# Kernel optimization log

Measured on AMD Instinct MI355X. Metric: run time of the kernel, lower is better.

Reference implementation:

```python
import jax, jax.numpy as jnp
import numpy as np

THRESH = 0.1        # Huber threshold (self.threshold)
CORR_WT = 1.0       # corr_wt
ENTROPY_WT = 0.0001 # entropy_wt
BS, N = 32, 1024    # n_pts = nv = 1024 hardcoded in multi_pose_with_pts


def setup_inputs() -> dict:
    key = jax.random.key(0)
    ks = jax.random.split(key, 7)
    return {
        "points_1": jax.random.normal(ks[0], (BS, N, 3), jnp.float32),
        "points_2": jax.random.normal(ks[1], (BS, N, 3), jnp.float32),
        "assign_mat_1": jax.random.normal(ks[2], (BS, N, N), jnp.float32),
        "assign_mat_2": jax.random.normal(ks[3], (BS, N, N), jnp.float32),
        "scale": jax.random.uniform(ks[4], (BS,), jnp.float32, 0.5, 1.5),
        "rotation": jax.random.normal(ks[5], (BS, 3, 3), jnp.float32),
        "translation": jax.random.normal(ks[6], (BS, 3), jnp.float32),
    }


def _transform(sRt, pts):
    # apply 4x4 pose to [b, n, 3] points (homogeneous, keep xyz)
    return jnp.einsum('bij,bnj->bni', sRt[:, :3, :3], pts) + sRt[:, :3, 3][:, None, :]


def _chamfer(x, y):
    # squared pairwise distances [b, n, m]; loss = mean min both directions
    d = (jnp.sum(x * x, -1)[:, :, None] + jnp.sum(y * y, -1)[:, None, :]
         - 2.0 * jnp.einsum('bnd,bmd->bnm', x, y))
    d = jnp.maximum(d, 0.0)
    return jnp.mean(jnp.min(d, axis=2)) + jnp.mean(jnp.min(d, axis=1))


def _corr(a, b):
    # smooth-L1-like (Huber) correspondence loss
    diff = jnp.abs(a - b)
    loss = jnp.where(diff > THRESH, diff - THRESH / 2.0, diff * diff / (2.0 * THRESH))
    return CORR_WT * jnp.mean(jnp.sum(loss, axis=2))


def _entropy(assign_mat, soft_assign, axis):
    log_assign = jax.nn.log_softmax(assign_mat, axis=axis)
    return ENTROPY_WT * jnp.mean(-jnp.sum(soft_assign * log_assign, axis=axis))


def _cos_loss(m1, m2, eps=1e-8):
    a = m1.reshape(m1.shape[0], -1)
    b = m2.reshape(m2.shape[0], -1)
    na = jnp.maximum(jnp.linalg.norm(a, axis=1), eps)
    nb = jnp.maximum(jnp.linalg.norm(b, axis=1), eps)
    return jnp.mean(1.0 - jnp.sum(a * b, axis=1) / (na * nb))


def reference(points_1, points_2, assign_mat_1, assign_mat_2, scale, rotation, translation):
    sa1 = jax.nn.softmax(assign_mat_1, axis=2)
    sa2 = jax.nn.softmax(assign_mat_2, axis=2)

    # pose_dict_RT: sRt = [[s*R, t], [0, 1]]
    sR = rotation * scale[:, None, None]
    sRt = jnp.concatenate([sR, translation[:, :, None]], axis=2)          # b 3 4
    bottom = jnp.broadcast_to(jnp.array([0., 0., 0., 1.], sRt.dtype), (sRt.shape[0], 1, 4))
    sRt12 = jnp.concatenate([sRt, bottom], axis=1)                        # b 4 4
    sRt21 = jnp.linalg.inv(sRt12)

    p1in2 = jnp.einsum('bnm,bmd->bnd', sa1, points_2)
    p2in1 = jnp.einsum('bnm,bmd->bnd', sa2, points_1)
    p1to2 = _transform(sRt12, points_1)
    p2to1 = _transform(sRt21, points_2)

    cd1 = _chamfer(p1to2, p1in2)
    cd2 = _chamfer(p2to1, p2in1)
    total = (cd1 + cd2
             + _corr(p1in2, p1to2) + _corr(p2in1, p2to1)
             + _entropy(assign_mat_1, sa1, 2) + _entropy(assign_mat_2, sa2, 2)
             + _cos_loss(assign_mat_1, assign_mat_2)
             + _entropy(assign_mat_1, sa1, 1) + _entropy(assign_mat_2, sa2, 1))
    return total
```

## Files before the change

kernel.cpp:

```cpp
#include <hip/hip_runtime.h>
#include <math.h>

#define BSZ 32
#define NP  1024

#define OFF_ACC   0
#define OFF_COS   8
#define OFF_POSE  104
#define OFF_P1IN2 872
#define OFF_P2IN1 (OFF_P1IN2 + 3 * BSZ * NP)
#define OFF_COLP  (OFF_P2IN1 + 3 * BSZ * NP)

__global__ void k_pose(const float* __restrict__ scale,
                       const float* __restrict__ rot,
                       const float* __restrict__ tr,
                       float* __restrict__ ws) {
    int t = threadIdx.x;
    if (t < 52) {
        ws[OFF_ACC + 2 * t]     = 0.f;
        ws[OFF_ACC + 2 * t + 1] = 0.f;
    }
    if (t >= BSZ) return;
    int b = t;
    float s = scale[b];
    float M[9];
#pragma unroll
    for (int i = 0; i < 9; ++i) M[i] = rot[b * 9 + i] * s;
    float t0 = tr[b * 3 + 0], t1 = tr[b * 3 + 1], t2 = tr[b * 3 + 2];
    float det = M[0] * (M[4] * M[8] - M[5] * M[7])
              - M[1] * (M[3] * M[8] - M[5] * M[6])
              + M[2] * (M[3] * M[7] - M[4] * M[6]);
    float id = 1.0f / det;
    float inv[9];
    inv[0] =  (M[4] * M[8] - M[5] * M[7]) * id;
    inv[1] = -(M[1] * M[8] - M[2] * M[7]) * id;
    inv[2] =  (M[1] * M[5] - M[2] * M[4]) * id;
    inv[3] = -(M[3] * M[8] - M[5] * M[6]) * id;
    inv[4] =  (M[0] * M[8] - M[2] * M[6]) * id;
    inv[5] = -(M[0] * M[5] - M[2] * M[3]) * id;
    inv[6] =  (M[3] * M[7] - M[4] * M[6]) * id;
    inv[7] = -(M[0] * M[7] - M[1] * M[6]) * id;
    inv[8] =  (M[0] * M[4] - M[1] * M[3]) * id;
    float u0 = -(inv[0] * t0 + inv[1] * t1 + inv[2] * t2);
    float u1 = -(inv[3] * t0 + inv[4] * t1 + inv[5] * t2);
    float u2 = -(inv[6] * t0 + inv[7] * t1 + inv[8] * t2);
    float* P = ws + OFF_POSE + b * 24;
#pragma unroll
    for (int i = 0; i < 9; ++i) P[i] = M[i];
    P[9] = t0; P[10] = t1; P[11] = t2;
#pragma unroll
    for (int i = 0; i < 9; ++i) P[12 + i] = inv[i];
    P[21] = u0; P[22] = u1; P[23] = u2;
}

__global__ __launch_bounds__(256) void k_big(
    const float* __restrict__ am1, const float* __restrict__ am2,
    const float* __restrict__ pts1, const float* __restrict__ pts2,
    float* __restrict__ p1in2, float* __restrict__ p2in1,
    float* __restrict__ colPart, float* __restrict__ cosacc, float* __restrict__ acc) {
    __shared__ float cacc[4096];
    __shared__ float ptsL[6144];
    const int b  = blockIdx.x >> 5;
    const int rb = blockIdx.x & 31;
    const int wv = threadIdx.x >> 6;
    const int ln = threadIdx.x & 63;
    const int row0 = rb * 32 + wv * 8;

    for (int i = threadIdx.x; i < 4096; i += 256) cacc[i] = 0.f;
    for (int t = threadIdx.x; t < 6144; t += 256) {
        int mat = t >= 3072;
        int loc = t - mat * 3072;
        int c = loc / 3, d = loc - 3 * c;
        float v = mat ? pts1[b * 3072 + loc] : pts2[b * 3072 + loc];
        ptsL[mat * 3072 + d * 1024 + 256 * (c & 3) + (c >> 2)] = v;
    }
    __syncthreads();

    float C1[16], T1[16], C2[16], T2[16];
#pragma unroll
    for (int i = 0; i < 16; ++i) { C1[i] = 0.f; T1[i] = 0.f; C2[i] = 0.f; T2[i] = 0.f; }
    float dacc = 0.f, n1a = 0.f, n2a = 0.f, e2a = 0.f, sSa = 0.f;

    const float4* rA = (const float4*)(am1 + ((size_t)b * NP + row0) * NP);
    const float4* rB = (const float4*)(am2 + ((size_t)b * NP + row0) * NP);

#pragma unroll 1
    for (int r = 0; r < 8; ++r) {
        float4 a[4], c4[4];
#pragma unroll
        for (int j = 0; j < 4; ++j) {
            a[j]  = rA[(size_t)r * 256 + ln + 64 * j];
            c4[j] = rB[(size_t)r * 256 + ln + 64 * j];
        }
#pragma unroll
        for (int j = 0; j < 4; ++j) {
            dacc += a[j].x * c4[j].x + a[j].y * c4[j].y + a[j].z * c4[j].z + a[j].w * c4[j].w;
            n1a  += a[j].x * a[j].x + a[j].y * a[j].y + a[j].z * a[j].z + a[j].w * a[j].w;
            n2a  += c4[j].x * c4[j].x + c4[j].y * c4[j].y + c4[j].z * c4[j].z + c4[j].w * c4[j].w;
        }
        {
            float R = 0.f, Su = 0.f, q0 = 0.f, q1 = 0.f, q2 = 0.f;
#pragma unroll
            for (int j = 0; j < 4; ++j) {
                float* e = (float*)&a[j];
#pragma unroll
                for (int k = 0; k < 4; ++k) {
                    int i = 4 * j + k;
                    int pidx = 256 * k + 64 * j + ln;
                    float v  = e[k];
                    float ex = __expf(v);
                    R += ex; Su += ex * v;
                    q0 += ex * ptsL[pidx];
                    q1 += ex * ptsL[1024 + pidx];
                    q2 += ex * ptsL[2048 + pidx];
                    C1[i] += ex;
                    e[k] = ex;
                }
            }
#pragma unroll
            for (int m = 1; m < 64; m <<= 1) {
                R  += __shfl_xor(R, m);  Su += __shfl_xor(Su, m);
                q0 += __shfl_xor(q0, m); q1 += __shfl_xor(q1, m); q2 += __shfl_xor(q2, m);
            }
            float inv = 1.0f / R;
#pragma unroll
            for (int j = 0; j < 4; ++j) {
                float* e = (float*)&a[j];
#pragma unroll
                for (int k = 0; k < 4; ++k) T1[4 * j + k] += e[k] * inv;
            }
            float S = Su * inv;
            if (ln == 0) {
                e2a += __logf(R) - S;
                sSa += S;
                int row = b * NP + row0 + r;
                p1in2[row * 3 + 0] = q0 * inv;
                p1in2[row * 3 + 1] = q1 * inv;
                p1in2[row * 3 + 2] = q2 * inv;
            }
        }
        {
            float R = 0.f, Su = 0.f, q0 = 0.f, q1 = 0.f, q2 = 0.f;
#pragma unroll
            for (int j = 0; j < 4; ++j) {
                float* e = (float*)&c4[j];
#pragma unroll
                for (int k = 0; k < 4; ++k) {
                    int i = 4 * j + k;
                    int pidx = 3072 + 256 * k + 64 * j + ln;
                    float v  = e[k];
                    float ex = __expf(v);
                    R += ex; Su += ex * v;
                    q0 += ex * ptsL[pidx];
                    q1 += ex * ptsL[1024 + pidx];
                    q2 += ex * ptsL[2048 + pidx];
                    C2[i] += ex;
                    e[k] = ex;
                }
            }
#pragma unroll
            for (int m = 1; m < 64; m <<= 1) {
                R  += __shfl_xor(R, m);  Su += __shfl_xor(Su, m);
                q0 += __shfl_xor(q0, m); q1 += __shfl_xor(q1, m); q2 += __shfl_xor(q2, m);
            }
            float inv = 1.0f / R;
#pragma unroll
            for (int j = 0; j < 4; ++j) {
                float* e = (float*)&c4[j];
#pragma unroll
                for (int k = 0; k < 4; ++k) T2[4 * j + k] += e[k] * inv;
            }
            float S = Su * inv;
            if (ln == 0) {
                e2a += __logf(R) - S;
                sSa += S;
                int row = b * NP + row0 + r;
                p2in1[row * 3 + 0] = q0 * inv;
                p2in1[row * 3 + 1] = q1 * inv;
                p2in1[row * 3 + 2] = q2 * inv;
            }
        }
    }

#pragma unroll
    for (int j = 0; j < 4; ++j)
#pragma unroll
        for (int k = 0; k < 4; ++k) {
            int i = 4 * j + k;
            int c = 256 * j + 4 * ln + k;
            atomicAdd(&cacc[c],        C1[i]);
            atomicAdd(&cacc[1024 + c], T1[i]);
            atomicAdd(&cacc[2048 + c], C2[i]);
            atomicAdd(&cacc[3072 + c], T2[i]);
        }
#pragma unroll
    for (int m = 1; m < 64; m <<= 1) {
        dacc += __shfl_xor(dacc, m);
        n1a  += __shfl_xor(n1a, m);
        n2a  += __shfl_xor(n2a, m);
    }
    if (ln == 0) {
        atomicAdd(&cosacc[b], dacc);
        atomicAdd(&cosacc[32 + b], n1a);
        atomicAdd(&cosacc[64 + b], n2a);
        atomicAdd(&acc[0], e2a);
        atomicAdd(&acc[1], sSa);
    }
    __syncthreads();
    float4* cp = (float4*)(colPart + (size_t)blockIdx.x * 4096);
    const float4* cs = (const float4*)cacc;
    for (int i = threadIdx.x; i < 1024; i += 256) cp[i] = cs[i];
}

__global__ void k_colred(const float* __restrict__ colPart, float* __restrict__ acc) {
    int idx = blockIdx.x * 256 + threadIdx.x;
    int b = idx >> 11;
    int m = (idx >> 10) & 1;
    int c = idx & 1023;
    const float* p = colPart + (size_t)b * 32 * 4096 + m * 2048 + c;
    float C = 0.f, T = 0.f;
#pragma unroll
    for (int rbi = 0; rbi < 32; ++rbi) {
        C += p[rbi * 4096];
        T += p[rbi * 4096 + 1024];
    }
    float v = T * __logf(C);
#pragma unroll
    for (int mm = 1; mm < 64; mm <<= 1) v += __shfl_xor(v, mm);
    if ((threadIdx.x & 63) == 0) atomicAdd(&acc[2], v);
}

__global__ __launch_bounds__(256) void k_cham(
    const float* __restrict__ p1, const float* __restrict__ p2,
    const float* __restrict__ p1in2, const float* __restrict__ p2in1,
    const float* __restrict__ pose, float* __restrict__ acc) {
    __shared__ float4 ys[NP];
    const int blk   = blockIdx.x;
    const int chunk = blk & 3;
    const int b     = (blk >> 2) & 31;
    const int dir   = (blk >> 7) & 1;
    const int pair  = blk >> 8;
    const float* P   = pose + b * 24 + pair * 12;
    const float* raw = pair ? p2 : p1;
    const float* inA = pair ? p2in1 : p1in2;
    const int t = threadIdx.x;

    float m0 = P[0], m1 = P[1], m2 = P[2];
    float m3 = P[3], m4 = P[4], m5 = P[5];
    float m6 = P[6], m7 = P[7], m8 = P[8];
    float t0 = P[9], t1 = P[10], t2 = P[11];

#pragma unroll
    for (int i = 0; i < 4; ++i) {
        int q = t + 256 * i;
        int gi = (b * NP + q) * 3;
        float x, y, z;
        if (dir == 0) { x = inA[gi]; y = inA[gi + 1]; z = inA[gi + 2]; }
        else {
            float rx = raw[gi], ry = raw[gi + 1], rz = raw[gi + 2];
            x = m0 * rx + m1 * ry + m2 * rz + t0;
            y = m3 * rx + m4 * ry + m5 * rz + t1;
            z = m6 * rx + m7 * ry + m8 * rz + t2;
        }
        ys[q] = make_float4(x, y, z, x * x + y * y + z * z);
    }
    __syncthreads();

    int xi = chunk * 256 + t;
    int gx = (b * NP + xi) * 3;
    float x0, x1, x2;
    if (dir == 0) {
        float rx = raw[gx], ry = raw[gx + 1], rz = raw[gx + 2];
        x0 = m0 * rx + m1 * ry + m2 * rz + t0;
        x1 = m3 * rx + m4 * ry + m5 * rz + t1;
        x2 = m6 * rx + m7 * ry + m8 * rz + t2;
    } else { x0 = inA[gx]; x1 = inA[gx + 1]; x2 = inA[gx + 2]; }
    float sx = x0 * x0 + x1 * x1 + x2 * x2;

    float mn = 3.0e38f;
#pragma unroll 4
    for (int o = 0; o < NP; ++o) {
        float4 yv = ys[o];
        float d = fmaf(-2.0f, x0 * yv.x + x1 * yv.y + x2 * yv.z, sx + yv.w);
        mn = fminf(mn, d);
    }
    mn = fmaxf(mn, 0.0f);

    float v = mn;
#pragma unroll
    for (int m = 1; m < 64; m <<= 1) v += __shfl_xor(v, m);
    if ((t & 63) == 0) atomicAdd(&acc[4], v);

    if (dir == 0) {
        float4 a = ys[xi];
        float s = 0.f;
        float d0 = fabsf(a.x - x0); s += (d0 > 0.1f) ? (d0 - 0.05f) : (d0 * d0 * 5.0f);
        float d1 = fabsf(a.y - x1); s += (d1 > 0.1f) ? (d1 - 0.05f) : (d1 * d1 * 5.0f);
        float d2 = fabsf(a.z - x2); s += (d2 > 0.1f) ? (d2 - 0.05f) : (d2 * d2 * 5.0f);
#pragma unroll
        for (int m = 1; m < 64; m <<= 1) s += __shfl_xor(s, m);
        if ((t & 63) == 0) atomicAdd(&acc[3], s);
    }
}

__global__ void k_final(const float* __restrict__ acc, const float* __restrict__ cosacc,
                        float* __restrict__ out) {
    if (threadIdx.x != 0) return;
    const float invBN = 1.0f / 32768.0f;
    float ent2 = 1e-4f * acc[0] * invBN;
    float ent1 = 1e-4f * (acc[2] - acc[1]) * invBN;
    float corr = acc[3] * invBN;
    float cham = acc[4] * invBN;
    float cosl = 0.f;
    for (int b = 0; b < 32; ++b) {
        float dot = cosacc[b];
        float na = fmaxf(sqrtf(cosacc[32 + b]), 1e-8f);
        float nb = fmaxf(sqrtf(cosacc[64 + b]), 1e-8f);
        cosl += 1.0f - dot / (na * nb);
    }
    cosl *= (1.0f / 32.0f);
    out[0] = cham + corr + ent2 + ent1 + cosl;
}

extern "C" void kernel_launch(void* const* d_in, const int* in_sizes, int n_in,
                              void* d_out, int out_size, void* d_ws, size_t ws_size,
                              hipStream_t stream) {
    const float* p1    = (const float*)d_in[0];
    const float* p2    = (const float*)d_in[1];
    const float* am1   = (const float*)d_in[2];
    const float* am2   = (const float*)d_in[3];
    const float* scale = (const float*)d_in[4];
    const float* rot   = (const float*)d_in[5];
    const float* tr    = (const float*)d_in[6];

    float* ws = (float*)d_ws;
    float* acc     = ws + OFF_ACC;
    float* cosacc  = ws + OFF_COS;
    float* pose    = ws + OFF_POSE;
    float* p1in2   = ws + OFF_P1IN2;
    float* p2in1   = ws + OFF_P2IN1;
    float* colPart = ws + OFF_COLP;

    k_pose<<<1, 64, 0, stream>>>(scale, rot, tr, ws);
    k_big<<<1024, 256, 0, stream>>>(am1, am2, p1, p2, p1in2, p2in1,
                                    colPart, cosacc, acc);
    k_colred<<<256, 256, 0, stream>>>(colPart, acc);
    k_cham<<<512, 256, 0, stream>>>(p1, p2, p1in2, p2in1, pose, acc);
    k_final<<<1, 64, 0, stream>>>(acc, cosacc, (float*)d_out);
}
```

Baseline: 547.4 us.

## Split fused row/column pass into separate row-softmax and column-reduction kernels

The single fused kernel that computed row softmax stats, column sums and the cosine terms is split into two kernels. A row kernel handles one matrix per block, keeping the point coordinates in registers, and writes the reciprocal row sums. A column kernel then re-reads both assignment matrices with a column-friendly layout, recomputing exp and accumulating per-column sums without shared-memory atomics. This removes the LDS atomics and register pressure of the fused version, but both 128 MB input matrices are now read twice from memory.

```diff
diff --git a/kernel.cpp b/kernel.cpp
--- a/kernel.cpp
+++ b/kernel.cpp
@@ -8,8 +8,9 @@
 #define OFF_COS   8
 #define OFF_POSE  104
 #define OFF_P1IN2 872
-#define OFF_P2IN1 (OFF_P1IN2 + 3 * BSZ * NP)
-#define OFF_COLP  (OFF_P2IN1 + 3 * BSZ * NP)
+#define OFF_P2IN1 (OFF_P1IN2 + 98304)
+#define OFF_INVR  (OFF_P2IN1 + 98304)
+#define OFF_COLP  (OFF_INVR + 65536)
 
 __global__ void k_pose(const float* __restrict__ scale,
                        const float* __restrict__ rot,
@@ -53,180 +54,155 @@
     P[21] = u0; P[22] = u1; P[23] = u2;
 }
 
-__global__ __launch_bounds__(256) void k_big(
+__global__ __launch_bounds__(256) void k_rows(
     const float* __restrict__ am1, const float* __restrict__ am2,
     const float* __restrict__ pts1, const float* __restrict__ pts2,
     float* __restrict__ p1in2, float* __restrict__ p2in1,
-    float* __restrict__ colPart, float* __restrict__ cosacc, float* __restrict__ acc) {
-    __shared__ float cacc[4096];
-    __shared__ float ptsL[6144];
-    const int b  = blockIdx.x >> 5;
-    const int rb = blockIdx.x & 31;
-    const int wv = threadIdx.x >> 6;
-    const int ln = threadIdx.x & 63;
+    float* __restrict__ invR, float* __restrict__ acc) {
+    __shared__ float sred[8];
+    const int bid = blockIdx.x;
+    const int rb = bid & 31;
+    const int m  = (bid >> 5) & 1;
+    const int b  = bid >> 6;
+    const int wv = threadIdx.x >> 6, ln = threadIdx.x & 63;
     const int row0 = rb * 32 + wv * 8;
-
-    for (int i = threadIdx.x; i < 4096; i += 256) cacc[i] = 0.f;
-    for (int t = threadIdx.x; t < 6144; t += 256) {
-        int mat = t >= 3072;
-        int loc = t - mat * 3072;
-        int c = loc / 3, d = loc - 3 * c;
-        float v = mat ? pts1[b * 3072 + loc] : pts2[b * 3072 + loc];
-        ptsL[mat * 3072 + d * 1024 + 256 * (c & 3) + (c >> 2)] = v;
-    }
-    __syncthreads();
-
-    float C1[16], T1[16], C2[16], T2[16];
-#pragma unroll
-    for (int i = 0; i < 16; ++i) { C1[i] = 0.f; T1[i] = 0.f; C2[i] = 0.f; T2[i] = 0.f; }
-    float dacc = 0.f, n1a = 0.f, n2a = 0.f, e2a = 0.f, sSa = 0.f;
-
-    const float4* rA = (const float4*)(am1 + ((size_t)b * NP + row0) * NP);
-    const float4* rB = (const float4*)(am2 + ((size_t)b * NP + row0) * NP);
+    const float* am  = m ? am2 : am1;
+    const float* pts = m ? pts1 : pts2;
+    float* pout   = m ? p2in1 : p1in2;
+    float* invout = invR + (m * BSZ + b) * NP;
+
+    float P[16][3];
+#pragma unroll
+    for (int j = 0; j < 4; ++j)
+#pragma unroll
+        for (int k = 0; k < 4; ++k) {
+            int c = 256 * j + 4 * ln + k;
+            const float* p = pts + ((size_t)b * NP + c) * 3;
+            P[4 * j + k][0] = p[0];
+            P[4 * j + k][1] = p[1];
+            P[4 * j + k][2] = p[2];
+        }
+
+    float e2a = 0.f, sSa = 0.f;
+    const float4* rA = (const float4*)(am + ((size_t)b * NP + row0) * NP);
 
 #pragma unroll 1
     for (int r = 0; r < 8; ++r) {
-        float4 a[4], c4[4];
+        float4 a[4];
+#pragma unroll
+        for (int j = 0; j < 4; ++j) a[j] = rA[(size_t)r * 256 + ln + 64 * j];
+        float R = 0.f, Su = 0.f, q0 = 0.f, q1 = 0.f, q2 = 0.f;
 #pragma unroll
         for (int j = 0; j < 4; ++j) {
-            a[j]  = rA[(size_t)r * 256 + ln + 64 * j];
-            c4[j] = rB[(size_t)r * 256 + ln + 64 * j];
-        }
-#pragma unroll
-        for (int j = 0; j < 4; ++j) {
-            dacc += a[j].x * c4[j].x + a[j].y * c4[j].y + a[j].z * c4[j].z + a[j].w * c4[j].w;
-            n1a  += a[j].x * a[j].x + a[j].y * a[j].y + a[j].z * a[j].z + a[j].w * a[j].w;
-            n2a  += c4[j].x * c4[j].x + c4[j].y * c4[j].y + c4[j].z * c4[j].z + c4[j].w * c4[j].w;
-        }
-        {
-            float R = 0.f, Su = 0.f, q0 = 0.f, q1 = 0.f, q2 = 0.f;
-#pragma unroll
-            for (int j = 0; j < 4; ++j) {
-                float* e = (float*)&a[j];
-#pragma unroll
-                for (int k = 0; k < 4; ++k) {
-                    int i = 4 * j + k;
-                    int pidx = 256 * k + 64 * j + ln;
-                    float v  = e[k];
-                    float ex = __expf(v);
-                    R += ex; Su += ex * v;
-                    q0 += ex * ptsL[pidx];
-                    q1 += ex * ptsL[1024 + pidx];
-                    q2 += ex * ptsL[2048 + pidx];
-                    C1[i] += ex;
-                    e[k] = ex;
-                }
+            float* e = (float*)&a[j];
+#pragma unroll
+            for (int k = 0; k < 4; ++k) {
+                int i = 4 * j + k;
+                float v  = e[k];
+                float ex = __expf(v);
+                R += ex; Su += ex * v;
+                q0 += ex * P[i][0]; q1 += ex * P[i][1]; q2 += ex * P[i][2];
             }
-#pragma unroll
-            for (int m = 1; m < 64; m <<= 1) {
-                R  += __shfl_xor(R, m);  Su += __shfl_xor(Su, m);
-                q0 += __shfl_xor(q0, m); q1 += __shfl_xor(q1, m); q2 += __shfl_xor(q2, m);
-            }
+        }
+#pragma unroll
+        for (int s = 1; s < 64; s <<= 1) {
+            R  += __shfl_xor(R, s);  Su += __shfl_xor(Su, s);
+            q0 += __shfl_xor(q0, s); q1 += __shfl_xor(q1, s); q2 += __shfl_xor(q2, s);
+        }
+        if (ln == 0) {
             float inv = 1.0f / R;
-#pragma unroll
-            for (int j = 0; j < 4; ++j) {
-                float* e = (float*)&a[j];
-#pragma unroll
-                for (int k = 0; k < 4; ++k) T1[4 * j + k] += e[k] * inv;
-            }
             float S = Su * inv;
-            if (ln == 0) {
-                e2a += __logf(R) - S;
-                sSa += S;
-                int row = b * NP + row0 + r;
-                p1in2[row * 3 + 0] = q0 * inv;
-                p1in2[row * 3 + 1] = q1 * inv;
-                p1in2[row * 3 + 2] = q2 * inv;
-            }
-        }
-        {
-            float R = 0.f, Su = 0.f, q0 = 0.f, q1 = 0.f, q2 = 0.f;
-#pragma unroll
-            for (int j = 0; j < 4; ++j) {
-                float* e = (float*)&c4[j];
-#pragma unroll
-                for (int k = 0; k < 4; ++k) {
-                    int i = 4 * j + k;
-                    int pidx = 3072 + 256 * k + 64 * j + ln;
-                    float v  = e[k];
-                    float ex = __expf(v);
-                    R += ex; Su += ex * v;
-                    q0 += ex * ptsL[pidx];
-                    q1 += ex * ptsL[1024 + pidx];
-                    q2 += ex * ptsL[2048 + pidx];
-                    C2[i] += ex;
-                    e[k] = ex;
-                }
-            }
-#pragma unroll
-            for (int m = 1; m < 64; m <<= 1) {
-                R  += __shfl_xor(R, m);  Su += __shfl_xor(Su, m);
-                q0 += __shfl_xor(q0, m); q1 += __shfl_xor(q1, m); q2 += __shfl_xor(q2, m);
-            }
-            float inv = 1.0f / R;
-#pragma unroll
-            for (int j = 0; j < 4; ++j) {
-                float* e = (float*)&c4[j];
-#pragma unroll
-                for (int k = 0; k < 4; ++k) T2[4 * j + k] += e[k] * inv;
-            }
-            float S = Su * inv;
-            if (ln == 0) {
-                e2a += __logf(R) - S;
-                sSa += S;
-                int row = b * NP + row0 + r;
-                p2in1[row * 3 + 0] = q0 * inv;
-                p2in1[row * 3 + 1] = q1 * inv;
-                p2in1[row * 3 + 2] = q2 * inv;
-            }
-        }
-    }
-
-#pragma unroll
-    for (int j = 0; j < 4; ++j)
-#pragma unroll
-        for (int k = 0; k < 4; ++k) {
-            int i = 4 * j + k;
-            int c = 256 * j + 4 * ln + k;
-            atomicAdd(&cacc[c],        C1[i]);
-            atomicAdd(&cacc[1024 + c], T1[i]);
-            atomicAdd(&cacc[2048 + c], C2[i]);
-            atomicAdd(&cacc[3072 + c], T2[i]);
-        }
-#pragma unroll
-    for (int m = 1; m < 64; m <<= 1) {
-        dacc += __shfl_xor(dacc, m);
-        n1a  += __shfl_xor(n1a, m);
-        n2a  += __shfl_xor(n2a, m);
-    }
-    if (ln == 0) {
-        atomicAdd(&cosacc[b], dacc);
-        atomicAdd(&cosacc[32 + b], n1a);
-        atomicAdd(&cosacc[64 + b], n2a);
-        atomicAdd(&acc[0], e2a);
-        atomicAdd(&acc[1], sSa);
-    }
+            e2a += __logf(R) - S;
+            sSa += S;
+            int row = row0 + r;
+            invout[row] = inv;
+            float* o = pout + ((size_t)b * NP + row) * 3;
+            o[0] = q0 * inv; o[1] = q1 * inv; o[2] = q2 * inv;
+        }
+    }
+    if (ln == 0) { sred[wv] = e2a; sred[4 + wv] = sSa; }
     __syncthreads();
-    float4* cp = (float4*)(colPart + (size_t)blockIdx.x * 4096);
-    const float4* cs = (const float4*)cacc;
-    for (int i = threadIdx.x; i < 1024; i += 256) cp[i] = cs[i];
-}
-
-__global__ void k_colred(const float* __restrict__ colPart, float* __restrict__ acc) {
+    if (threadIdx.x == 0) {
+        atomicAdd(&acc[0], sred[0] + sred[1] + sred[2] + sred[3]);
+        atomicAdd(&acc[1], sred[4] + sred[5] + sred[6] + sred[7]);
+    }
+}
+
+__global__ __launch_bounds__(256) void k_cols2(
+    const float* __restrict__ am1, const float* __restrict__ am2,
+    const float* __restrict__ invR, float* __restrict__ colP,
+    float* __restrict__ cosacc) {
+    __shared__ float invL[64];
+    __shared__ float cred[12];
+    const int rt = blockIdx.x & 31;
+    const int b  = blockIdx.x >> 5;
+    const int t  = threadIdx.x;
+    if (t < 64) {
+        int mm = t >> 5, rr = t & 31;
+        invL[t] = invR[(mm * BSZ + b) * NP + rt * 32 + rr];
+    }
+    __syncthreads();
+    const float4* s1 = (const float4*)(am1 + ((size_t)b * NP + rt * 32) * NP) + t;
+    const float4* s2 = (const float4*)(am2 + ((size_t)b * NP + rt * 32) * NP) + t;
+    float C1x=0,C1y=0,C1z=0,C1w=0, T1x=0,T1y=0,T1z=0,T1w=0;
+    float C2x=0,C2y=0,C2z=0,C2w=0, T2x=0,T2y=0,T2z=0,T2w=0;
+    float dacc = 0.f, n1a = 0.f, n2a = 0.f;
+#pragma unroll 4
+    for (int r = 0; r < 32; ++r) {
+        float4 v1 = s1[(size_t)r * 256];
+        float4 v2 = s2[(size_t)r * 256];
+        dacc += v1.x*v2.x + v1.y*v2.y + v1.z*v2.z + v1.w*v2.w;
+        n1a  += v1.x*v1.x + v1.y*v1.y + v1.z*v1.z + v1.w*v1.w;
+        n2a  += v2.x*v2.x + v2.y*v2.y + v2.z*v2.z + v2.w*v2.w;
+        float w1 = invL[r], w2 = invL[32 + r];
+        float e;
+        e = __expf(v1.x); C1x += e; T1x += e * w1;
+        e = __expf(v1.y); C1y += e; T1y += e * w1;
+        e = __expf(v1.z); C1z += e; T1z += e * w1;
+        e = __expf(v1.w); C1w += e; T1w += e * w1;
+        e = __expf(v2.x); C2x += e; T2x += e * w2;
+        e = __expf(v2.y); C2y += e; T2y += e * w2;
+        e = __expf(v2.z); C2z += e; T2z += e * w2;
+        e = __expf(v2.w); C2w += e; T2w += e * w2;
+    }
+    float4* cp = (float4*)colP + ((size_t)(b * 32 + rt)) * 1024 + t;
+    cp[0]   = make_float4(C1x, C1y, C1z, C1w);
+    cp[256] = make_float4(T1x, T1y, T1z, T1w);
+    cp[512] = make_float4(C2x, C2y, C2z, C2w);
+    cp[768] = make_float4(T2x, T2y, T2z, T2w);
+#pragma unroll
+    for (int s = 1; s < 64; s <<= 1) {
+        dacc += __shfl_xor(dacc, s);
+        n1a  += __shfl_xor(n1a, s);
+        n2a  += __shfl_xor(n2a, s);
+    }
+    if ((t & 63) == 0) {
+        int wv = t >> 6;
+        cred[wv] = dacc; cred[4 + wv] = n1a; cred[8 + wv] = n2a;
+    }
+    __syncthreads();
+    if (t == 0) {
+        atomicAdd(&cosacc[b],      cred[0] + cred[1] + cred[2]  + cred[3]);
+        atomicAdd(&cosacc[32 + b], cred[4] + cred[5] + cred[6]  + cred[7]);
+        atomicAdd(&cosacc[64 + b], cred[8] + cred[9] + cred[10] + cred[11]);
+    }
+}
+
+__global__ void k_colred2(const float* __restrict__ colP, float* __restrict__ acc) {
     int idx = blockIdx.x * 256 + threadIdx.x;
-    int b = idx >> 11;
-    int m = (idx >> 10) & 1;
-    int c = idx & 1023;
-    const float* p = colPart + (size_t)b * 32 * 4096 + m * 2048 + c;
+    int bm = idx >> 10;
+    int c  = idx & 1023;
+    int b = bm >> 1, m = bm & 1;
+    const float* base = colP + (size_t)b * 32 * 4 * NP + (2 * m) * NP + c;
     float C = 0.f, T = 0.f;
 #pragma unroll
-    for (int rbi = 0; rbi < 32; ++rbi) {
-        C += p[rbi * 4096];
-        T += p[rbi * 4096 + 1024];
+    for (int rt = 0; rt < 32; ++rt) {
+        C += base[(size_t)rt * 4 * NP];
+        T += base[(size_t)rt * 4 * NP + NP];
     }
     float v = T * __logf(C);
 #pragma unroll
-    for (int mm = 1; mm < 64; mm <<= 1) v += __shfl_xor(v, mm);
+    for (int s = 1; s < 64; s <<= 1) v += __shfl_xor(v, s);
     if ((threadIdx.x & 63) == 0) atomicAdd(&acc[2], v);
 }
 
@@ -334,17 +310,18 @@
     const float* tr    = (const float*)d_in[6];
 
     float* ws = (float*)d_ws;
-    float* acc     = ws + OFF_ACC;
-    float* cosacc  = ws + OFF_COS;
-    float* pose    = ws + OFF_POSE;
-    float* p1in2   = ws + OFF_P1IN2;
-    float* p2in1   = ws + OFF_P2IN1;
-    float* colPart = ws + OFF_COLP;
+    float* acc    = ws + OFF_ACC;
+    float* cosacc = ws + OFF_COS;
+    float* pose   = ws + OFF_POSE;
+    float* p1in2  = ws + OFF_P1IN2;
+    float* p2in1  = ws + OFF_P2IN1;
+    float* invR   = ws + OFF_INVR;
+    float* colP   = ws + OFF_COLP;
 
     k_pose<<<1, 64, 0, stream>>>(scale, rot, tr, ws);
-    k_big<<<1024, 256, 0, stream>>>(am1, am2, p1, p2, p1in2, p2in1,
-                                    colPart, cosacc, acc);
-    k_colred<<<256, 256, 0, stream>>>(colPart, acc);
+    k_rows<<<2048, 256, 0, stream>>>(am1, am2, p1, p2, p1in2, p2in1, invR, acc);
+    k_cols2<<<1024, 256, 0, stream>>>(am1, am2, invR, colP, cosacc);
+    k_colred2<<<256, 256, 0, stream>>>(colP, acc);
     k_cham<<<512, 256, 0, stream>>>(p1, p2, p1in2, p2in1, pose, acc);
     k_final<<<1, 64, 0, stream>>>(acc, cosacc, (float*)d_out);
 }
```

After: 470.9 us. 14.0% less time.
